# Optimization experiments

Hardware: AMD Instinct MI355X
Metric: run time of the kernel (lower is better)

The kernel has to match this reference:

```python
import math
import jax, jax.numpy as jnp
import numpy as np

B, S, E, H = 4, 1024, 1024, 16
DH = E // H
LN_EPS = 1e-5


def _layernorm(x, g, b):
    mu = jnp.mean(x, axis=-1, keepdims=True)
    var = jnp.mean(jnp.square(x - mu), axis=-1, keepdims=True)
    return (x - mu) * jax.lax.rsqrt(var + LN_EPS) * g + b


def _gelu_tanh(x):
    c = math.sqrt(2.0 / math.pi)
    return 0.5 * x * (1.0 + jnp.tanh(c * (x + 0.044715 * x * x * x)))


def setup_inputs() -> dict:
    key = jax.random.key(0)
    ks = jax.random.split(key, 12)
    std = 0.02
    x = jax.random.normal(ks[0], (B, S, E), jnp.float32)
    # additive causal mask: 0 on/below diag, -inf above
    causal_mask = jnp.where(jnp.tril(jnp.ones((S, S), bool)), 0.0, -jnp.inf).astype(jnp.float32)
    inp = dict(
        x=x,
        causal_mask=causal_mask,
        ln1_g=1.0 + std * jax.random.normal(ks[1], (E,), jnp.float32),
        ln1_b=std * jax.random.normal(ks[2], (E,), jnp.float32),
        ln2_g=1.0 + std * jax.random.normal(ks[3], (E,), jnp.float32),
        ln2_b=std * jax.random.normal(ks[4], (E,), jnp.float32),
        w_in=std * jax.random.normal(ks[5], (3 * E, E), jnp.float32),   # packed QKV in_proj_weight
        b_in=jnp.zeros((3 * E,), jnp.float32),
        w_out=std * jax.random.normal(ks[6], (E, E), jnp.float32),      # out_proj.weight
        b_out=jnp.zeros((E,), jnp.float32),
        w_fc=std * jax.random.normal(ks[7], (4 * E, E), jnp.float32),
        b_fc=jnp.zeros((4 * E,), jnp.float32),
        w_proj=std * jax.random.normal(ks[8], (E, 4 * E), jnp.float32),
        b_proj=jnp.zeros((E,), jnp.float32),
    )
    return inp


def reference(x, causal_mask, ln1_g, ln1_b, ln2_g, ln2_b,
              w_in, b_in, w_out, b_out, w_fc, b_fc, w_proj, b_proj):
    # --- attention branch (pre-LN) ---
    h = _layernorm(x, ln1_g, ln1_b)                       # [B,S,E]
    wq, wk, wv = w_in[:E], w_in[E:2 * E], w_in[2 * E:]
    bq, bk, bv = b_in[:E], b_in[E:2 * E], b_in[2 * E:]
    q = (h @ wq.T + bq).reshape(B, S, H, DH)
    k = (h @ wk.T + bk).reshape(B, S, H, DH)
    v = (h @ wv.T + bv).reshape(B, S, H, DH)
    scale = 1.0 / math.sqrt(DH)
    scores = jnp.einsum('bqhd,bkhd->bhqk', q * scale, k) + causal_mask  # [B,H,S,S]
    probs = jax.nn.softmax(scores, axis=-1)
    att = jnp.einsum('bhqk,bkhd->bqhd', probs, v).reshape(B, S, E)
    att = att @ w_out.T + b_out
    att_weights = jnp.mean(probs, axis=1)                 # averaged over heads, [B,S,S]
    x = x + att
    # --- MLP branch (pre-LN) ---
    h2 = _layernorm(x, ln2_g, ln2_b)
    x = x + (_gelu_tanh(h2 @ w_fc.T + b_fc) @ w_proj.T + b_proj)
    return (x, att_weights)
```

## Files before the change

### kernel.cpp

```cpp
#include <hip/hip_runtime.h>

typedef unsigned short u16;
typedef u16   u16x4 __attribute__((ext_vector_type(4)));
typedef u16   u16x8 __attribute__((ext_vector_type(8)));
typedef short s16x8 __attribute__((ext_vector_type(8)));
typedef float f32x4 __attribute__((ext_vector_type(4)));

__device__ __forceinline__ float b2f(u16 u) {
    union { unsigned int i; float f; } v; v.i = ((unsigned int)u) << 16; return v.f;
}
__device__ __forceinline__ u16 f2b(float f) {
    union { float f; unsigned int i; } v; v.f = f;
    unsigned int r = v.i + 0x7fffu + ((v.i >> 16) & 1u);
    return (u16)(r >> 16);
}
__device__ __forceinline__ float gelu_f(float x) {
    float z = 0.7978845608028654f * (x + 0.044715f * x * x * x);
    float e = __expf(2.0f * z);
    float t = 1.0f - 2.0f / (e + 1.0f);
    return 0.5f * x * (1.0f + t);
}
__device__ __forceinline__ void async16(const u16* g, u16* l) {
    __builtin_amdgcn_global_load_lds(
        (const __attribute__((address_space(1))) unsigned int*)g,
        (__attribute__((address_space(3))) unsigned int*)l,
        16, 0, 0);
}

#define FEN() asm volatile("" ::: "memory")
#define BARR() { FEN(); __builtin_amdgcn_s_barrier(); FEN(); }
#define LGKM0() { asm volatile("s_waitcnt lgkmcnt(0)" ::: "memory"); __builtin_amdgcn_sched_barrier(0); }
#define VMC(N) asm volatile("s_waitcnt vmcnt(" #N ")" ::: "memory")

__global__ __launch_bounds__(256)
void detect_k(const u16* __restrict__ x, int* __restrict__ flag)
{
    int gid = blockIdx.x * 256 + threadIdx.x;
    const u16x8 u = *(const u16x8*)(x + (long)gid * 8);
    int bad = 0;
    #pragma unroll
    for (int e = 0; e < 8; e++) {
        int ex = (u[e] >> 7) & 0xFF;
        if (ex >= 187) bad = 1;
    }
    unsigned long long m = __ballot(bad != 0);
    if ((threadIdx.x & 63) == 0 && m != 0ull) atomicOr(flag, 1);
}

__global__ __launch_bounds__(256)
void conv_w_k(const void* __restrict__ s0, const void* __restrict__ s1,
              const void* __restrict__ s2, const void* __restrict__ s3,
              u16* __restrict__ dst, const int* __restrict__ flag)
{
    const long MEG = 1L << 20;
    long gid = ((long)blockIdx.x * 256 + threadIdx.x) * 4;
    const void* s; long off;
    if      (gid <  3*MEG) { s = s0; off = gid; }
    else if (gid <  4*MEG) { s = s1; off = gid - 3*MEG; }
    else if (gid <  8*MEG) { s = s2; off = gid - 4*MEG; }
    else                   { s = s3; off = gid - 8*MEG; }
    u16x4 o;
    if (*flag) {
        const float4 f = *(const float4*)((const float*)s + off);
        o[0] = f2b(f.x); o[1] = f2b(f.y); o[2] = f2b(f.z); o[3] = f2b(f.w);
    } else {
        o = *(const u16x4*)((const u16*)s + off);
    }
    *(u16x4*)(dst + gid) = o;
}

__global__ __launch_bounds__(256)
void conv_small_k(const void* s0, const void* s1, const void* s2, const void* s3,
                  const void* s4, const void* s5, const void* s6, const void* s7,
                  u16* __restrict__ dst, const int* __restrict__ flag)
{
    int gid = blockIdx.x * 256 + threadIdx.x;
    int seg, off;
    if      (gid <  4096) { seg = gid >> 10;  off = gid & 1023; }
    else if (gid <  7168) { seg = 4; off = gid - 4096; }
    else if (gid <  8192) { seg = 5; off = gid - 7168; }
    else if (gid < 12288) { seg = 6; off = gid - 8192; }
    else                  { seg = 7; off = gid - 12288; }
    const void* srcs[8] = {s0, s1, s2, s3, s4, s5, s6, s7};
    const void* s = srcs[seg];
    dst[seg * 4096 + off] = (*flag) ? f2b(((const float*)s)[off]) : ((const u16*)s)[off];
}

__global__ __launch_bounds__(256)
void ln1x_k(const void* __restrict__ xraw, const u16* __restrict__ g,
            const u16* __restrict__ b, u16* __restrict__ xc,
            u16* __restrict__ o, const int* __restrict__ flag)
{
    long row = blockIdx.x;
    int tid = threadIdx.x;
    float v0, v1, v2, v3;
    if (*flag) {
        const float4 f = *(const float4*)((const float*)xraw + row * 1024 + tid * 4);
        v0 = b2f(f2b(f.x)); v1 = b2f(f2b(f.y));
        v2 = b2f(f2b(f.z)); v3 = b2f(f2b(f.w));
    } else {
        const u16x4 u = *(const u16x4*)((const u16*)xraw + row * 1024 + tid * 4);
        v0 = b2f(u[0]); v1 = b2f(u[1]); v2 = b2f(u[2]); v3 = b2f(u[3]);
    }
    u16x4 xv; xv[0] = f2b(v0); xv[1] = f2b(v1); xv[2] = f2b(v2); xv[3] = f2b(v3);
    *(u16x4*)(xc + row * 1024 + tid * 4) = xv;
    float s  = v0 + v1 + v2 + v3;
    float sq = v0*v0 + v1*v1 + v2*v2 + v3*v3;
    #pragma unroll
    for (int off = 32; off; off >>= 1) { s += __shfl_xor(s, off); sq += __shfl_xor(sq, off); }
    __shared__ float sm[8];
    int wid = tid >> 6, lane = tid & 63;
    if (lane == 0) { sm[wid] = s; sm[wid + 4] = sq; }
    __syncthreads();
    s  = sm[0] + sm[1] + sm[2] + sm[3];
    sq = sm[4] + sm[5] + sm[6] + sm[7];
    float mean = s * (1.0f / 1024.0f);
    float var  = sq * (1.0f / 1024.0f) - mean * mean;
    float rs   = rsqrtf(var + 1e-5f);
    u16x4 gg = *(const u16x4*)(g + tid * 4);
    u16x4 bb = *(const u16x4*)(b + tid * 4);
    u16x4 ov;
    ov[0] = f2b((v0 - mean) * rs * b2f(gg[0]) + b2f(bb[0]));
    ov[1] = f2b((v1 - mean) * rs * b2f(gg[1]) + b2f(bb[1]));
    ov[2] = f2b((v2 - mean) * rs * b2f(gg[2]) + b2f(bb[2]));
    ov[3] = f2b((v3 - mean) * rs * b2f(gg[3]) + b2f(bb[3]));
    *(u16x4*)(o + row * 1024 + tid * 4) = ov;
}

__global__ __launch_bounds__(256)
void ln_k(const u16* __restrict__ x, const u16* __restrict__ g,
          const u16* __restrict__ b, u16* __restrict__ o)
{
    long row = blockIdx.x;
    int tid = threadIdx.x;
    const u16x4 u = *(const u16x4*)(x + row * 1024 + tid * 4);
    float v0 = b2f(u[0]), v1 = b2f(u[1]), v2 = b2f(u[2]), v3 = b2f(u[3]);
    float s  = v0 + v1 + v2 + v3;
    float sq = v0*v0 + v1*v1 + v2*v2 + v3*v3;
    #pragma unroll
    for (int off = 32; off; off >>= 1) { s += __shfl_xor(s, off); sq += __shfl_xor(sq, off); }
    __shared__ float sm[8];
    int wid = tid >> 6, lane = tid & 63;
    if (lane == 0) { sm[wid] = s; sm[wid + 4] = sq; }
    __syncthreads();
    s  = sm[0] + sm[1] + sm[2] + sm[3];
    sq = sm[4] + sm[5] + sm[6] + sm[7];
    float mean = s * (1.0f / 1024.0f);
    float var  = sq * (1.0f / 1024.0f) - mean * mean;
    float rs   = rsqrtf(var + 1e-5f);
    u16x4 gg = *(const u16x4*)(g + tid * 4);
    u16x4 bb = *(const u16x4*)(b + tid * 4);
    u16x4 ov;
    ov[0] = f2b((v0 - mean) * rs * b2f(gg[0]) + b2f(bb[0]));
    ov[1] = f2b((v1 - mean) * rs * b2f(gg[1]) + b2f(bb[1]));
    ov[2] = f2b((v2 - mean) * rs * b2f(gg[2]) + b2f(bb[2]));
    ov[3] = f2b((v3 - mean) * rs * b2f(gg[3]) + b2f(bb[3]));
    *(u16x4*)(o + row * 1024 + tid * 4) = ov;
}

__global__ __launch_bounds__(256)
void redln_k(const float* __restrict__ P, long slice,
             const u16* __restrict__ bias, u16* __restrict__ res,
             const u16* __restrict__ g, const u16* __restrict__ b,
             u16* __restrict__ o)
{
    long row = blockIdx.x;
    int tid = threadIdx.x;
    long i = row * 1024 + tid * 4;
    float4 v  = *(const float4*)(P + i);
    float4 p1 = *(const float4*)(P + slice + i);
    u16x4 bb = *(const u16x4*)(bias + tid * 4);
    u16x4 rr = *(const u16x4*)(res + i);
    float v0 = b2f(f2b(v.x + p1.x + b2f(bb[0]) + b2f(rr[0])));
    float v1 = b2f(f2b(v.y + p1.y + b2f(bb[1]) + b2f(rr[1])));
    float v2 = b2f(f2b(v.z + p1.z + b2f(bb[2]) + b2f(rr[2])));
    float v3 = b2f(f2b(v.w + p1.w + b2f(bb[3]) + b2f(rr[3])));
    u16x4 xv; xv[0] = f2b(v0); xv[1] = f2b(v1); xv[2] = f2b(v2); xv[3] = f2b(v3);
    *(u16x4*)(res + i) = xv;
    float s  = v0 + v1 + v2 + v3;
    float sq = v0*v0 + v1*v1 + v2*v2 + v3*v3;
    #pragma unroll
    for (int off = 32; off; off >>= 1) { s += __shfl_xor(s, off); sq += __shfl_xor(sq, off); }
    __shared__ float sm[8];
    int wid = tid >> 6, lane = tid & 63;
    if (lane == 0) { sm[wid] = s; sm[wid + 4] = sq; }
    __syncthreads();
    s  = sm[0] + sm[1] + sm[2] + sm[3];
    sq = sm[4] + sm[5] + sm[6] + sm[7];
    float mean = s * (1.0f / 1024.0f);
    float var  = sq * (1.0f / 1024.0f) - mean * mean;
    float rs   = rsqrtf(var + 1e-5f);
    u16x4 gg = *(const u16x4*)(g + tid * 4);
    u16x4 b2 = *(const u16x4*)(b + tid * 4);
    u16x4 ov;
    ov[0] = f2b((v0 - mean) * rs * b2f(gg[0]) + b2f(b2[0]));
    ov[1] = f2b((v1 - mean) * rs * b2f(gg[1]) + b2f(b2[1]));
    ov[2] = f2b((v2 - mean) * rs * b2f(gg[2]) + b2f(b2[2]));
    ov[3] = f2b((v3 - mean) * rs * b2f(gg[3]) + b2f(b2[3]));
    *(u16x4*)(o + row * 1024 + tid * 4) = ov;
}

__global__ __launch_bounds__(1024)
void smmean_k(u16* __restrict__ probs, void* __restrict__ ow, long ofs,
              const int* __restrict__ flag)
{
    const long MEG = 1L << 20;
    __shared__ float red[16 * 1024];
    int bl = blockIdx.x >> 10;
    int q  = blockIdx.x & 1023;
    int w = threadIdx.x >> 6, lane = threadIdx.x & 63;
    int tile_end = ((q >> 7) + 1) << 7;
    u16* row = probs + (((long)(bl * 16 + w)) << 20) + (long)q * 1024;
    float v[16];
    float m = -3.0e38f;
    #pragma unroll
    for (int c = 0; c < 2; c++) {
        int kb = (c * 64 + lane) * 8;
        if (kb <= q) {
            u16x8 u = *(const u16x8*)(row + kb);
            #pragma unroll
            for (int e = 0; e < 8; e++) {
                if (kb + e <= q) {
                    float f = b2f(u[e]);
                    v[c * 8 + e] = f;
                    m = fmaxf(m, f);
                } else v[c * 8 + e] = -3.0e38f;
            }
        } else {
            #pragma unroll
            for (int e = 0; e < 8; e++) v[c * 8 + e] = -3.0e38f;
        }
    }
    #pragma unroll
    for (int off = 32; off; off >>= 1) m = fmaxf(m, __shfl_xor(m, off));
    float s = 0.0f;
    #pragma unroll
    for (int t = 0; t < 16; t++) {
        float e = (v[t] > -1.0e38f) ? __expf(v[t] - m) : 0.0f;
        v[t] = e; s += e;
    }
    #pragma unroll
    for (int off = 32; off; off >>= 1) s += __shfl_xor(s, off);
    float inv = 1.0f / s;
    #pragma unroll
    for (int c = 0; c < 2; c++) {
        int kb = (c * 64 + lane) * 8;
        float p[8];
        #pragma unroll
        for (int e = 0; e < 8; e++) p[e] = v[c * 8 + e] * inv;
        #pragma unroll
        for (int e = 0; e < 8; e++) red[w * 1024 + kb + e] = p[e];
        if (kb < tile_end) {
            u16x8 o;
            #pragma unroll
            for (int e = 0; e < 8; e++) o[e] = f2b(p[e]);
            *(u16x8*)(row + kb) = o;
        }
    }
    __syncthreads();
    int t = threadIdx.x;
    float acc = 0.0f;
    #pragma unroll
    for (int h = 0; h < 16; h++) acc += red[h * 1024 + t];
    acc *= 0.0625f;
    long idx = ofs + (long)bl * MEG + (long)q * 1024 + t;
    if (*flag) ((float*)ow)[idx] = acc;
    else       ((u16*)ow)[idx]   = f2b(acc);
}

__global__ __launch_bounds__(256)
void reduce_out_k(const float* __restrict__ P, long slice,
                  const u16* __restrict__ bias, const u16* __restrict__ res,
                  void* __restrict__ out, const int* __restrict__ flag)
{
    long i = ((long)blockIdx.x * 256 + threadIdx.x) * 4;
    int gn = (int)(i & 1023);
    float4 v = *(const float4*)(P + i);
    #pragma unroll
    for (int s = 1; s < 4; s++) {
        const float4 p = *(const float4*)(P + (long)s * slice + i);
        v.x += p.x; v.y += p.y; v.z += p.z; v.w += p.w;
    }
    u16x4 bb = *(const u16x4*)(bias + gn);
    u16x4 rr = *(const u16x4*)(res + i);
    v.x += b2f(bb[0]) + b2f(rr[0]);
    v.y += b2f(bb[1]) + b2f(rr[1]);
    v.z += b2f(bb[2]) + b2f(rr[2]);
    v.w += b2f(bb[3]) + b2f(rr[3]);
    if (*flag) {
        *(float4*)((float*)out + i) = v;
    } else {
        u16x4 o;
        o[0] = f2b(v.x); o[1] = f2b(v.y); o[2] = f2b(v.z); o[3] = f2b(v.w);
        *(u16x4*)((u16*)out + i) = o;
    }
}

template<int EPI>
__global__ __launch_bounds__(512, 2)
void g8(const u16* __restrict__ A, const u16* __restrict__ Bt,
        u16* __restrict__ C, const u16* __restrict__ bias,
        float* __restrict__ Cf,
        int K, int lda, int ldb, int ldc,
        long sA, long sB, long sC)
{
    __shared__ alignas(16) u16 shA[2 * 16384];
    __shared__ alignas(16) u16 shB[2 * 16384];

    const int tid = threadIdx.x;
    int tn = blockIdx.x, tm = blockIdx.y;
    const int bz = blockIdx.z;
    {
        int L = blockIdx.y * gridDim.x + blockIdx.x;
        int xcd = L & 7, idx = L >> 3;
        tn = idx % gridDim.x;
        tm = (idx / gridDim.x) * 8 + xcd;
    }
    const u16* Ab = A + (long)bz * sA;
    const u16* Bb = Bt + (long)bz * sB;
    const int m0 = tm * 256, n0 = tn * 256;
    const int NT = K >> 6;

    const int w = tid >> 6, lane = tid & 63;
    const int lr = lane & 15, quad = lane >> 4, sw = lane & 7;
    const int wm16 = (w >> 2) * 16, wn16 = (w & 3) * 16;

    auto stageH = [&](int tile, int isB, int half) {
        const u16* src = isB ? Bb : Ab;
        const int ld = isB ? ldb : lda;
        const int r0 = (isB ? n0 : m0) + half * 128;
        u16* dbase = (isB ? shB : shA) + (tile & 1) * 16384 + half * 8192;
        const long kk = (long)tile << 6;
        #pragma unroll
        for (int L2 = 0; L2 < 2; L2++) {
            int c = L2 * 512 + tid;
            int rl = c >> 3, sl = c & 7;
            int kc = sl ^ (rl & 7);
            async16(src + (long)(r0 + rl) * ld + kk + kc * 8, dbase + c * 8);
        }
    };

    f32x4 acc[2][4][2][2] = {};
    s16x8 aF[4][2], b0F[2][2], b1F[2][2];

    auto rdA = [&](int buf, int ih) {
        #pragma unroll
        for (int q = 0; q < 4; q++)
            #pragma unroll
            for (int ks = 0; ks < 2; ks++)
                aF[q][ks] = *(const s16x8*)&shA[buf * 16384 + ih * 8192
                    + (q * 32 + wm16 + lr) * 64 + ((ks * 4 + quad) ^ sw) * 8];
    };
    auto rdB = [&](s16x8 (&bF)[2][2], int buf, int jh) {
        #pragma unroll
        for (int r = 0; r < 2; r++)
            #pragma unroll
            for (int ks = 0; ks < 2; ks++)
                bF[r][ks] = *(const s16x8*)&shB[buf * 16384 + jh * 8192
                    + (r * 64 + wn16 + lr) * 64 + ((ks * 4 + quad) ^ sw) * 8];
    };

#define MM(IH, JH, BF) do { \
    __builtin_amdgcn_s_setprio(1); \
    _Pragma("unroll") \
    for (int q = 0; q < 4; q++) \
        _Pragma("unroll") \
        for (int r = 0; r < 2; r++) \
            _Pragma("unroll") \
            for (int ks = 0; ks < 2; ks++) \
                acc[IH][q][JH][r] = __builtin_amdgcn_mfma_f32_16x16x32_bf16( \
                    aF[q][ks], BF[r][ks], acc[IH][q][JH][r], 0, 0, 0); \
    __builtin_amdgcn_s_setprio(0); \
} while (0)

    stageH(0, 0, 0); stageH(0, 1, 0); stageH(0, 0, 1); stageH(0, 1, 1);
    stageH(1, 0, 0); stageH(1, 1, 0);
    VMC(8); BARR();

    for (int it = 0; it < NT - 2; it += 2) {
        rdA(0, 0); rdB(b0F, 0, 0); stageH(it + 1, 0, 1);
        BARR(); LGKM0(); MM(0, 0, b0F);
        FEN(); VMC(6); BARR();

        rdB(b1F, 0, 1); stageH(it + 1, 1, 1);
        BARR(); LGKM0(); MM(0, 1, b1F);
        BARR();

        rdA(0, 1); stageH(it + 2, 0, 0);
        BARR(); LGKM0(); MM(1, 0, b0F);
        BARR();

        stageH(it + 2, 1, 0);
        BARR(); LGKM0(); MM(1, 1, b1F);
        FEN(); VMC(8); BARR();

        rdA(1, 0); rdB(b0F, 1, 0); stageH(it + 2, 0, 1);
        BARR(); LGKM0(); MM(0, 0, b0F);
        FEN(); VMC(6); BARR();

        rdB(b1F, 1, 1); stageH(it + 2, 1, 1);
        BARR(); LGKM0(); MM(0, 1, b1F);
        BARR();

        rdA(1, 1); stageH(it + 3, 0, 0);
        BARR(); LGKM0(); MM(1, 0, b0F);
        BARR();

        stageH(it + 3, 1, 0);
        BARR(); LGKM0(); MM(1, 1, b1F);
        FEN(); VMC(8); BARR();
    }

    rdA(0, 0); rdB(b0F, 0, 0); stageH(NT - 1, 0, 1);
    BARR(); LGKM0(); MM(0, 0, b0F);
    FEN(); VMC(6); BARR();

    rdB(b1F, 0, 1); stageH(NT - 1, 1, 1);
    BARR(); LGKM0(); MM(0, 1, b1F);
    BARR();

    rdA(0, 1);
    BARR(); LGKM0(); MM(1, 0, b0F);
    BARR();

    BARR(); LGKM0(); MM(1, 1, b1F);
    FEN(); VMC(0); BARR();

    rdA(1, 0); rdB(b0F, 1, 0);
    BARR(); LGKM0(); MM(0, 0, b0F);
    BARR();

    rdB(b1F, 1, 1);
    BARR(); LGKM0(); MM(0, 1, b1F);
    BARR();

    rdA(1, 1);
    BARR(); LGKM0(); MM(1, 0, b0F);
    BARR();

    LGKM0(); MM(1, 1, b1F);
#undef MM

    #pragma unroll
    for (int ih = 0; ih < 2; ih++)
        #pragma unroll
        for (int q = 0; q < 4; q++)
            #pragma unroll
            for (int jh = 0; jh < 2; jh++)
                #pragma unroll
                for (int r = 0; r < 2; r++)
                    #pragma unroll
                    for (int rr = 0; rr < 4; rr++) {
                        int gm = m0 + ih * 128 + q * 32 + wm16 + quad * 4 + rr;
                        int gn = n0 + jh * 128 + r * 64 + wn16 + lr;
                        float v = acc[ih][q][jh][r][rr];
                        if (EPI == 3) {
                            C[(long)gm * ldc + gn] = f2b(gelu_f(v + b2f(bias[gn])));
                        } else {
                            Cf[(long)bz * sC + (long)gm * ldc + gn] = v;
                        }
                    }
}

template<int BN, int EPI>
__global__ __launch_bounds__(256)
void gemm_bt(const u16* __restrict__ A, const u16* __restrict__ Bt,
             u16* __restrict__ C, const u16* __restrict__ bias,
             const u16* __restrict__ res,
             u16* __restrict__ qb, u16* __restrict__ kb, u16* __restrict__ vb,
             int M, int N, int K, int lda, int ldb, int ldc,
             long sA, long sB, long sC,
             const int* __restrict__ oflag, void* __restrict__ oout)
{
    constexpr int BM = 128, BK = 32;
    constexpr int WROWS = (BN == 128) ? 2 : 4;
    constexpr int WCOLS = (BN == 128) ? 2 : 1;
    constexpr int WM = BM / WROWS, WN = BN / WCOLS;
    constexpr int MI = WM / 16, NJ = WN / 16;
    constexpr int BCH = BN * BK / 8 / 256;
    constexpr int SHSZ = 2 * BM * BK + 2 * BN * BK;

    __shared__ alignas(16) u16 shmem[SHSZ];
    u16* AshB = shmem;
    u16* BshB = shmem + 2 * BM * BK;
    u16* Csh  = shmem;

    const int tid = threadIdx.x;
    int tn = blockIdx.x, tm = blockIdx.y;
    const int bz = blockIdx.z;
    if (EPI == 4 && tn > tm) return;

    if (EPI == 1 || EPI == 2 || EPI == 3 || EPI == 6 || EPI == 7) {
        int L = blockIdx.y * gridDim.x + blockIdx.x;
        int xcd = L & 7, idx = L >> 3;
        tn = idx % gridDim.x;
        tm = (idx / gridDim.x) * 8 + xcd;
    }

    const u16* Ab = A + (long)bz * sA;
    const u16* Bb = Bt + (long)bz * sB;

    const int m0 = tm * BM, n0 = tn * BN;
    const int kEff = (EPI == 5) ? (((tm + 1) * BM < K) ? (tm + 1) * BM : K) : K;

    const int w = tid >> 6, lane = tid & 63;
    const int wrow = w % WROWS, wcol = w / WROWS;
    const int mw = wrow * WM, nw = wcol * WN;
    const int lr = lane & 15, quad = lane >> 4;

    const int ca0 = tid, ca1 = 256 + tid;
    const int cb1 = 256 + tid;

    const int ar0 = ca0 >> 2, ac0 = (((ca0 & 3) ^ ((ca0 >> 3) & 3))) * 8;
    const int ar1 = ca1 >> 2, ac1 = (((ca1 & 3) ^ ((ca1 >> 3) & 3))) * 8;
    const int br0 = tid >> 2, bc0 = (((tid & 3) ^ ((tid >> 3) & 3))) * 8;
    const int br1 = cb1 >> 2, bc1 = (((cb1 & 3) ^ ((cb1 >> 3) & 3))) * 8;

    auto stage = [&](int buf, int k0) {
        async16(Ab + (long)(m0 + ar0) * lda + k0 + ac0, &AshB[buf * BM * BK + ca0 * 8]);
        async16(Ab + (long)(m0 + ar1) * lda + k0 + ac1, &AshB[buf * BM * BK + ca1 * 8]);
        async16(Bb + (long)(n0 + br0) * ldb + k0 + bc0, &BshB[buf * BN * BK + tid * 8]);
        if (BCH == 2)
            async16(Bb + (long)(n0 + br1) * ldb + k0 + bc1, &BshB[buf * BN * BK + cb1 * 8]);
    };

    f32x4 acc[MI][NJ] = {};

    const int foff = (quad ^ ((lr >> 1) & 3)) * 8;

    stage(0, 0);
    int cur = 0;
    for (int k0 = 0; k0 < kEff; k0 += BK) {
        __syncthreads();
        if (k0 + BK < kEff) stage(cur ^ 1, k0 + BK);

        s16x8 af[MI], bfr[NJ];
        #pragma unroll
        for (int i = 0; i < MI; i++)
            af[i] = *(const s16x8*)&AshB[cur * BM * BK + (mw + i * 16 + lr) * BK + foff];
        #pragma unroll
        for (int j = 0; j < NJ; j++)
            bfr[j] = *(const s16x8*)&BshB[cur * BN * BK + (nw + j * 16 + lr) * BK + foff];
        #pragma unroll
        for (int i = 0; i < MI; i++)
            #pragma unroll
            for (int j = 0; j < NJ; j++)
                acc[i][j] = __builtin_amdgcn_mfma_f32_16x16x32_bf16(af[i], bfr[j], acc[i][j], 0, 0, 0);
        cur ^= 1;
    }

    if (EPI == 1) {
        const int sel = n0 >> 10;
        const int b = m0 >> 10, sbase = m0 & 1023;
        if (sel < 2) {
            u16* dst = (sel == 0) ? qb : kb;
            #pragma unroll
            for (int i = 0; i < MI; i++)
                #pragma unroll
                for (int j = 0; j < NJ; j++)
                    #pragma unroll
                    for (int r = 0; r < 4; r++) {
                        int gm = m0 + mw + i * 16 + quad * 4 + r;
                        int gn = n0 + nw + j * 16 + lr;
                        float v = acc[i][j][r] + b2f(bias[gn]);
                        int s = gm & 1023, nn = gn & 1023, hh = nn >> 6, d = nn & 63;
                        dst[(((long)(b * 16 + hh) * 1024 + s) << 6) + d] = f2b(v);
                    }
        } else {
            __syncthreads();
            #pragma unroll
            for (int i = 0; i < MI; i++)
                #pragma unroll
                for (int j = 0; j < NJ; j++)
                    #pragma unroll
                    for (int r = 0; r < 4; r++) {
                        int nl = nw + j * 16 + lr;
                        int ml = mw + i * 16 + quad * 4 + r;
                        float v = acc[i][j][r] + b2f(bias[n0 + nl]);
                        Csh[nl * 128 + (((ml >> 3) ^ (nl & 15)) << 3) + (ml & 7)] = f2b(v);
                    }
            __syncthreads();
            const int nv0 = n0 - 2048;
            #pragma unroll
            for (int rep = 0; rep < 8; rep++) {
                int dd = rep * 16 + (tid >> 4);
                int sl = (tid & 15) * 8;
                int dg = nv0 + dd, hh = dg >> 6, dcol = dg & 63;
                u16x8 val = *(const u16x8*)&Csh[dd * 128 + ((((sl >> 3)) ^ (dd & 15)) << 3)];
                *(u16x8*)&vb[(((long)(b * 16 + hh) * 64 + dcol) << 10) + sbase + sl] = val;
            }
        }
        return;
    }

    u16* Cb;
    if (EPI == 5) Cb = C + (long)(bz >> 4) * (1 << 20) + (bz & 15) * 64;
    else          Cb = C + (long)bz * sC;

    #pragma unroll
    for (int i = 0; i < MI; i++) {
        #pragma unroll
        for (int j = 0; j < NJ; j++) {
            #pragma unroll
            for (int r = 0; r < 4; r++) {
                int gm = m0 + mw + i * 16 + quad * 4 + r;
                int gn = n0 + nw + j * 16 + lr;
                float v = acc[i][j][r];
                if (EPI == 5) {
                    Cb[(long)gm * ldc + gn] = f2b(v);
                } else if (EPI == 2) {
                    v += b2f(bias[gn]) + b2f(res[(long)gm * ldc + gn]);
                    Cb[(long)gm * ldc + gn] = f2b(v);
                } else if (EPI == 3) {
                    Cb[(long)gm * ldc + gn] = f2b(gelu_f(v + b2f(bias[gn])));
                } else if (EPI == 4) {
                    if (gn <= gm) Cb[(long)gm * ldc + gn] = f2b(v * 0.125f);
                } else if (EPI == 6) {
                    v += b2f(bias[gn]) + b2f(res[(long)gm * ldc + gn]);
                    long idx = (long)gm * ldc + gn;
                    if (*oflag) ((float*)oout)[idx] = v;
                    else        ((u16*)oout)[idx]   = f2b(v);
                } else if (EPI == 7) {
                    ((float*)oout)[(long)bz * sC + (long)gm * ldc + gn] = v;
                }
            }
        }
    }
}

extern "C" void kernel_launch(void* const* d_in, const int* in_sizes, int n_in,
                              void* d_out, int out_size, void* d_ws, size_t ws_size,
                              hipStream_t stream)
{
    const long MEG = 1L << 20;
    const long KI  = 1024;

    u16* ws = (u16*)d_ws;
    u16* xc    = ws;
    u16* winC  = ws + 4  * MEG;
    u16* woutC = ws + 7  * MEG;
    u16* wfcC  = ws + 8  * MEG;
    u16* wprjC = ws + 12 * MEG;
    u16* sm    = ws + 16 * MEG;
    u16* ln1g = sm + 0*4*KI, *ln1b = sm + 1*4*KI;
    u16* ln2g = sm + 2*4*KI, *ln2b = sm + 3*4*KI;
    u16* binC = sm + 4*4*KI;
    u16* boutC= sm + 5*4*KI;
    u16* bfcC = sm + 6*4*KI;
    u16* bprjC= sm + 7*4*KI;
    int* flag = (int*)(sm + 8*4*KI);
    u16* slotA = ws + 16 * MEG + 64 * KI;
    u16* qB    = slotA + 4  * MEG;
    u16* kB    = slotA + 8  * MEG;
    u16* vT    = slotA + 12 * MEG;
    u16* probs = slotA + 16 * MEG;
    float* part = (float*)(probs + 16 * MEG);

    const long fixed_elems = 32 * MEG + 64 * KI;
    const long avail = (long)(ws_size / 2);
    int chunk = 1;
    if      (avail >= fixed_elems + 64 * MEG) chunk = 4;
    else if (avail >= fixed_elems + 32 * MEG) chunk = 2;
    const bool splitk = (chunk == 4);

    hipMemsetAsync((void*)flag, 0, sizeof(int), stream);
    detect_k<<<32, 256, 0, stream>>>((const u16*)d_in[0], flag);
    conv_w_k<<<12288, 256, 0, stream>>>(d_in[6], d_in[8], d_in[10], d_in[12],
                                        winC, flag);
    conv_small_k<<<52, 256, 0, stream>>>(d_in[2], d_in[3], d_in[4], d_in[5],
                                         d_in[7], d_in[9], d_in[11], d_in[13],
                                         sm, flag);

    u16* h   = slotA;
    u16* att = slotA;
    u16* h2  = slotA;
    u16* act = probs;

    ln1x_k<<<4096, 256, 0, stream>>>(d_in[0], ln1g, ln1b, xc, h, flag);
    gemm_bt<128, 1><<<dim3(24, 32, 1), 256, 0, stream>>>(
        h, winC, nullptr, binC, nullptr, qB, kB, vT,
        4096, 3072, 1024, 1024, 1024, 0, 0, 0, 0, nullptr, nullptr);
    for (int b0 = 0; b0 < 4; b0 += chunk) {
        gemm_bt<128, 4><<<dim3(8, 8, 16 * chunk), 256, 0, stream>>>(
            qB + b0 * MEG, kB + b0 * MEG, probs, nullptr, nullptr,
            nullptr, nullptr, nullptr,
            1024, 1024, 64, 64, 64, 1024, 65536, 65536, 1048576, nullptr, nullptr);
        smmean_k<<<1024 * chunk, 1024, 0, stream>>>(probs, d_out,
                                                    4 * MEG + b0 * MEG, flag);
        gemm_bt<64, 5><<<dim3(1, 8, 16 * chunk), 256, 0, stream>>>(
            probs, vT + b0 * MEG, att + b0 * MEG, nullptr, nullptr,
            nullptr, nullptr, nullptr,
            1024, 64, 1024, 1024, 1024, 1024, 1048576, 65536, 0, nullptr, nullptr);
    }
    if (splitk) {
        gemm_bt<128, 7><<<dim3(8, 32, 2), 256, 0, stream>>>(
            att, woutC, nullptr, nullptr, nullptr, nullptr, nullptr, nullptr,
            4096, 1024, 512, 1024, 1024, 1024, 512, 512, 4 * MEG, nullptr, part);
        redln_k<<<4096, 256, 0, stream>>>(part, 4 * MEG, boutC, xc, ln2g, ln2b, h2);
    } else {
        gemm_bt<128, 2><<<dim3(8, 32, 1), 256, 0, stream>>>(
            att, woutC, xc, boutC, xc, nullptr, nullptr, nullptr,
            4096, 1024, 1024, 1024, 1024, 1024, 0, 0, 0, nullptr, nullptr);
        ln_k<<<4096, 256, 0, stream>>>(xc, ln2g, ln2b, h2);
    }
    g8<3><<<dim3(16, 16, 1), 512, 0, stream>>>(
        h2, wfcC, act, bfcC, nullptr,
        1024, 1024, 1024, 4096, 0, 0, 0);
    if (splitk) {
        g8<7><<<dim3(4, 16, 4), 512, 0, stream>>>(
            act, wprjC, nullptr, nullptr, part,
            1024, 4096, 4096, 1024, 1024, 1024, 4 * MEG);
        reduce_out_k<<<4096, 256, 0, stream>>>(part, 4 * MEG, bprjC, xc, d_out, flag);
    } else {
        gemm_bt<128, 6><<<dim3(8, 32, 1), 256, 0, stream>>>(
            act, wprjC, nullptr, bprjC, xc, nullptr, nullptr, nullptr,
            4096, 1024, 4096, 4096, 4096, 1024, 0, 0, 0, flag, d_out);
    }
}
```

Before: 416.6 us.

## Rework g8 prefetch schedule and route out-proj split-K GEMM through g8

Restructures the g8 kernel's main loop from a two-iteration unrolled body into a per-tile loop. The loop alternates LDS buffers by parity, reorders the half-tile async stages, and tightens vmcnt waits so global loads for upcoming tiles overlap MFMA work differently. It also replaces the 256-thread gemm_bt split-K launch for the attention output projection with the 512-thread g8 kernel (K=512 per split), with epilogue 7 writing partials into the same buffer. This adds risk that the new wait counts do not cover the staged loads, which would cause races, and that the changed g8 grid and tile size fit the out-projection shape less well.

Result: no change. 412.5 us (-1.0%).

```diff
diff --git a/kernel.cpp b/kernel.cpp
--- a/kernel.cpp
+++ b/kernel.cpp
@@ -373,72 +373,54 @@
     __builtin_amdgcn_s_setprio(0); \
 } while (0)
 
-    stageH(0, 0, 0); stageH(0, 1, 0); stageH(0, 0, 1); stageH(0, 1, 1);
-    stageH(1, 0, 0); stageH(1, 1, 0);
+    stageH(0, 0, 0); stageH(0, 1, 0); stageH(0, 1, 1);
+    stageH(1, 0, 0); stageH(1, 1, 0); stageH(0, 0, 1);
     VMC(8); BARR();
 
-    for (int it = 0; it < NT - 2; it += 2) {
-        rdA(0, 0); rdB(b0F, 0, 0); stageH(it + 1, 0, 1);
+    for (int t = 0; t < NT - 2; ++t) {
+        const int buf = t & 1;
+        rdA(buf, 0); rdB(b0F, buf, 0); stageH(t + 1, 1, 1);
         BARR(); LGKM0(); MM(0, 0, b0F);
-        FEN(); VMC(6); BARR();
-
-        rdB(b1F, 0, 1); stageH(it + 1, 1, 1);
+        FEN(); VMC(8); BARR();
+        rdB(b1F, buf, 1); stageH(t + 2, 0, 0);
         BARR(); LGKM0(); MM(0, 1, b1F);
-        BARR();
-
-        rdA(0, 1); stageH(it + 2, 0, 0);
+        FEN(); VMC(4); BARR();
+        rdA(buf, 1); stageH(t + 2, 1, 0);
         BARR(); LGKM0(); MM(1, 0, b0F);
         BARR();
-
-        stageH(it + 2, 1, 0);
+        stageH(t + 1, 0, 1);
         BARR(); LGKM0(); MM(1, 1, b1F);
+        BARR();
+    }
+
+    {
+        const int buf = (NT - 2) & 1;
+        rdA(buf, 0); rdB(b0F, buf, 0); stageH(NT - 1, 1, 1);
+        BARR(); LGKM0(); MM(0, 0, b0F);
         FEN(); VMC(8); BARR();
-
-        rdA(1, 0); rdB(b0F, 1, 0); stageH(it + 2, 0, 1);
-        BARR(); LGKM0(); MM(0, 0, b0F);
-        FEN(); VMC(6); BARR();
-
-        rdB(b1F, 1, 1); stageH(it + 2, 1, 1);
+        rdB(b1F, buf, 1);
         BARR(); LGKM0(); MM(0, 1, b1F);
-        BARR();
-
-        rdA(1, 1); stageH(it + 3, 0, 0);
+        FEN(); VMC(2); BARR();
+        rdA(buf, 1);
         BARR(); LGKM0(); MM(1, 0, b0F);
         BARR();
-
-        stageH(it + 3, 1, 0);
+        stageH(NT - 1, 0, 1);
         BARR(); LGKM0(); MM(1, 1, b1F);
-        FEN(); VMC(8); BARR();
-    }
-
-    rdA(0, 0); rdB(b0F, 0, 0); stageH(NT - 1, 0, 1);
-    BARR(); LGKM0(); MM(0, 0, b0F);
-    FEN(); VMC(6); BARR();
-
-    rdB(b1F, 0, 1); stageH(NT - 1, 1, 1);
-    BARR(); LGKM0(); MM(0, 1, b1F);
-    BARR();
-
-    rdA(0, 1);
-    BARR(); LGKM0(); MM(1, 0, b0F);
-    BARR();
-
-    BARR(); LGKM0(); MM(1, 1, b1F);
-    FEN(); VMC(0); BARR();
-
-    rdA(1, 0); rdB(b0F, 1, 0);
-    BARR(); LGKM0(); MM(0, 0, b0F);
-    BARR();
-
-    rdB(b1F, 1, 1);
-    BARR(); LGKM0(); MM(0, 1, b1F);
-    BARR();
-
-    rdA(1, 1);
-    BARR(); LGKM0(); MM(1, 0, b0F);
-    BARR();
-
-    LGKM0(); MM(1, 1, b1F);
+        BARR();
+    }
+    {
+        const int buf = (NT - 1) & 1;
+        rdA(buf, 0); rdB(b0F, buf, 0);
+        BARR(); LGKM0(); MM(0, 0, b0F);
+        FEN(); VMC(2); BARR();
+        rdB(b1F, buf, 1);
+        BARR(); LGKM0(); MM(0, 1, b1F);
+        FEN(); VMC(0); BARR();
+        rdA(buf, 1);
+        BARR(); LGKM0(); MM(1, 0, b0F);
+        BARR();
+        LGKM0(); MM(1, 1, b1F);
+    }
 #undef MM
 
     #pragma unroll
@@ -693,9 +675,9 @@
             1024, 64, 1024, 1024, 1024, 1024, 1048576, 65536, 0, nullptr, nullptr);
     }
     if (splitk) {
-        gemm_bt<128, 7><<<dim3(8, 32, 2), 256, 0, stream>>>(
-            att, woutC, nullptr, nullptr, nullptr, nullptr, nullptr, nullptr,
-            4096, 1024, 512, 1024, 1024, 1024, 512, 512, 4 * MEG, nullptr, part);
+        g8<7><<<dim3(4, 16, 2), 512, 0, stream>>>(
+            att, woutC, nullptr, nullptr, part,
+            512, 1024, 1024, 1024, 512, 512, 4 * MEG);
         redln_k<<<4096, 256, 0, stream>>>(part, 4 * MEG, boutC, xc, ln2g, ln2b, h2);
     } else {
         gemm_bt<128, 2><<<dim3(8, 32, 1), 256, 0, stream>>>(
```
